# Performance work log

Measured on AMD Instinct MI355X. Metric: run time of the kernel, lower is better.

## Reference

```python
import jax, jax.numpy as jnp
import numpy as np

MARGIN = 0.075
CONF_THRESHOLD = 0.2


def setup_inputs() -> dict:
    key = jax.random.key(0)
    k1, k2, k3 = jax.random.split(key, 3)
    N, D = 32768, 256
    embeddings = jax.random.normal(k1, (N, D), dtype=jnp.float32)
    tags = jax.random.randint(k2, (N,), 0, 500, dtype=jnp.int64)
    confidences = jax.random.uniform(k3, (N,), dtype=jnp.float32)
    return {"embeddings": embeddings, "tags": tags, "confidences": confidences}


def _safe_sqrt(sq):
    # gradient-safe sqrt: zero at sq<=0 (matches d(0)=0, avoids NaN in vjp)
    pos = sq > 0
    return jnp.where(pos, jnp.sqrt(jnp.where(pos, sq, 1.0)), 0.0)


def _triplet_hard_mining(emb, labels):
    n = emb.shape[0]
    # pairwise euclidean distances (cdist p=2)
    sq_norm = jnp.sum(emb * emb, axis=1)  # [n]
    sq = sq_norm[:, None] + sq_norm[None, :] - 2.0 * (emb @ emb.T)
    dist = _safe_sqrt(jnp.maximum(sq, 0.0))  # [n, n]

    same = labels[:, None] == labels[None, :]
    eye = jnp.eye(n, dtype=bool)
    pos_mask = same & ~eye
    neg_mask = ~same

    inf = jnp.float32(jnp.inf)
    hard_pos = jnp.max(jnp.where(pos_mask, dist, -inf), axis=1)  # [n]
    neg_min = jnp.min(jnp.where(neg_mask, dist, inf), axis=1)    # [n]
    # semi-hard negatives: neg dists strictly greater than hardest positive
    shn_mask = neg_mask & (dist > hard_pos[:, None])
    shn_min = jnp.min(jnp.where(shn_mask, dist, inf), axis=1)
    hard_neg = jnp.where(jnp.isfinite(shn_min), shn_min, neg_min)

    valid = jnp.any(pos_mask, axis=1) & jnp.any(neg_mask, axis=1)
    per_anchor = jax.nn.relu(hard_pos - hard_neg + MARGIN)
    per_anchor = jnp.where(valid, per_anchor, 0.0)
    cnt = jnp.sum(valid.astype(jnp.float32))
    # if no valid anchors (also covers <2 unique labels), loss is 0
    return jnp.where(cnt > 0, jnp.sum(per_anchor) / jnp.maximum(cnt, 1.0), 0.0)


def reference(embeddings, tags, confidences):
    n = embeddings.shape[0]
    top_k = int(CONF_THRESHOLD * n)
    _, idx = jax.lax.top_k(confidences, top_k)
    emb = embeddings[idx]
    labels = tags[idx]
    return _triplet_hard_mining(emb, labels)
```

## Files before the change

kernel.cpp:

```cpp
#include <hip/hip_runtime.h>
#include <math.h>

#define D 256
#define MARGIN 0.075f
#define MAXM 96
#define NBIN 16384

typedef __bf16 bf8_t __attribute__((ext_vector_type(8)));
typedef float f4_t __attribute__((ext_vector_type(4)));
typedef unsigned long long ull;

#define AS1 __attribute__((address_space(1)))
#define AS3 __attribute__((address_space(3)))
static __device__ __forceinline__ void gload_lds16(const void* g, void* s) {
    __builtin_amdgcn_global_load_lds((const AS1 unsigned int*)g, (AS3 unsigned int*)s, 16, 0, 0);
}

#define ALOADU(p) __hip_atomic_load((p), __ATOMIC_RELAXED, __HIP_MEMORY_SCOPE_AGENT)
#define ASTOREU(p, v) __hip_atomic_store((p), (v), __ATOMIC_RELAXED, __HIP_MEMORY_SCOPE_AGENT)

#define VDRAIN() asm volatile("s_waitcnt vmcnt(0)" ::: "memory")

static __device__ __forceinline__ unsigned short f2bf(float x) {
    unsigned u = __float_as_uint(x);
    unsigned r = (u + 0x7fffu + ((u >> 16) & 1u)) >> 16;
    return (unsigned short)r;
}

static __device__ __forceinline__ float dec_min(unsigned cm) {
    return (cm == 0u) ? __builtin_inff() : __uint_as_float(~cm);
}

static __device__ __forceinline__ float rmin16(float v) {
    int s;
    s = __builtin_amdgcn_update_dpp(__float_as_int(v), __float_as_int(v), 0x101, 0xF, 0xF, false);
    v = fminf(v, __int_as_float(s));
    s = __builtin_amdgcn_update_dpp(__float_as_int(v), __float_as_int(v), 0x102, 0xF, 0xF, false);
    v = fminf(v, __int_as_float(s));
    s = __builtin_amdgcn_update_dpp(__float_as_int(v), __float_as_int(v), 0x104, 0xF, 0xF, false);
    v = fminf(v, __int_as_float(s));
    s = __builtin_amdgcn_update_dpp(__float_as_int(v), __float_as_int(v), 0x108, 0xF, 0xF, false);
    v = fminf(v, __int_as_float(s));
    return v;
}

__global__ __launch_bounds__(1024) void k_hist(const float* __restrict__ conf, int n,
                                               unsigned* __restrict__ hist,
                                               unsigned* __restrict__ ctrl, int ksel) {
    int t = threadIdx.x;
    int i = blockIdx.x * 1024 + t;
    if (i < n) {
        unsigned b = __float_as_uint(conf[i]) >> 16;
        if (b > NBIN - 1u) b = NBIN - 1u;
        atomicAdd(&hist[b], 1u);
    }
    VDRAIN();
    __syncthreads();
    __shared__ int lastf;
    if (t == 0) lastf = (atomicAdd(&ctrl[10], 1u) == gridDim.x - 1) ? 1 : 0;
    __syncthreads();
    if (!lastf) return;

    __shared__ unsigned part[1024];
    __shared__ int schunk;
    unsigned k = (unsigned)ksel;
    unsigned loc[16];
    unsigned s = 0;
    #pragma unroll
    for (int b = 0; b < 16; b++) {
        loc[b] = ALOADU(&hist[t * 16 + b]);
        s += loc[b];
    }
    part[t] = s;
    __syncthreads();
    for (int off = 1; off < 1024; off <<= 1) {
        unsigned v = (t + off < 1024) ? part[t + off] : 0u;
        __syncthreads();
        part[t] += v;
        __syncthreads();
    }
    if (part[t] >= k && (t == 1023 || part[t + 1] < k)) schunk = t;
    __syncthreads();
    int c = schunk;
    if (t == c) {
        unsigned cum = (c == 1023) ? 0u : part[c + 1];
        int bin = 0; unsigned rem = 1;
        #pragma unroll
        for (int b = 15; b >= 0; b--) {
            unsigned h = loc[b];
            if (cum + h >= k) { bin = c * 16 + b; rem = k - cum; break; }
            cum += h;
        }
        ctrl[3] = (unsigned)bin;
        ctrl[1] = k - rem;
        ctrl[2] = rem;
    }
}

__global__ __launch_bounds__(1024) void k_sel(const float* __restrict__ conf, int n,
                                              unsigned* __restrict__ ctrl,
                                              int* __restrict__ idx_sel,
                                              ull* __restrict__ cand) {
    int t = threadIdx.x;
    int i = blockIdx.x * 1024 + t;
    unsigned b16 = ctrl[3];
    if (i < n) {
        unsigned u = __float_as_uint(conf[i]);
        unsigned t16 = u >> 16;
        if (t16 > NBIN - 1u) t16 = NBIN - 1u;
        if (t16 > b16) {
            unsigned pos = atomicAdd(&ctrl[5], 1u);
            idx_sel[pos] = i;
        } else if (t16 == b16) {
            unsigned pos = atomicAdd(&ctrl[6], 1u);
            ASTOREU(&cand[pos], ((ull)u << 32) | (unsigned)i);
        }
    }
    VDRAIN();
    __syncthreads();
    __shared__ int lastf;
    if (t == 0) lastf = (atomicAdd(&ctrl[11], 1u) == gridDim.x - 1) ? 1 : 0;
    __syncthreads();
    if (!lastf) return;

    __shared__ ull scand[2048];
    int M = (int)ALOADU(&ctrl[6]);
    unsigned need = ctrl[2], cgt = ctrl[1];
    if (M <= 2048) {
        for (int j = t; j < M; j += 1024) scand[j] = ALOADU(&cand[j]);
        __syncthreads();
        for (int j = t; j < M; j += 1024) {
            ull cj = scand[j];
            unsigned uj = (unsigned)(cj >> 32);
            unsigned rank = 0;
            for (int m = 0; m < M; m++) {
                ull cm = scand[m];
                unsigned um = (unsigned)(cm >> 32);
                if (um > uj || (um == uj && cm < cj)) rank++;
            }
            if (rank < need) idx_sel[cgt + rank] = (int)(unsigned)(cj & 0xFFFFFFFFu);
        }
    } else {
        for (int j = t; j < M; j += 1024) {
            ull cj = ALOADU(&cand[j]);
            unsigned uj = (unsigned)(cj >> 32);
            unsigned rank = 0;
            for (int m = 0; m < M; m++) {
                ull cm = ALOADU(&cand[m]);
                unsigned um = (unsigned)(cm >> 32);
                if (um > uj || (um == uj && cm < cj)) rank++;
            }
            if (rank < need) idx_sel[cgt + rank] = (int)(unsigned)(cj & 0xFFFFFFFFu);
        }
    }
}

__global__ __launch_bounds__(256) void k_gather(const float* __restrict__ emb,
                                                const int* __restrict__ tags,
                                                const int* __restrict__ idx_sel,
                                                int ksel, int np,
                                                unsigned short* __restrict__ ebf,
                                                float* __restrict__ sqn,
                                                int* __restrict__ lsel,
                                                unsigned* __restrict__ labhist,
                                                int* __restrict__ members) {
    int j = blockIdx.x * 4 + (threadIdx.x >> 6);
    int t = threadIdx.x & 63;
    if (j < ksel) {
        int src = idx_sel[j];
        float4 v = *(const float4*)&emb[(size_t)src * D + t * 4];
        ushort4 o;
        o.x = f2bf(v.x); o.y = f2bf(v.y); o.z = f2bf(v.z); o.w = f2bf(v.w);
        *(ushort4*)&ebf[(size_t)j * D + t * 4] = o;
        float s = v.x * v.x + v.y * v.y + v.z * v.z + v.w * v.w;
        for (int off = 32; off > 0; off >>= 1) s += __shfl_down(s, off);
        if (t == 0) {
            int lab = tags[src];
            sqn[j] = s; lsel[j] = lab;
            unsigned slot = atomicAdd(&labhist[lab], 1u);
            if (slot < MAXM) members[lab * MAXM + slot] = j;
        }
    } else if (j < np) {
        ushort4 z = {0, 0, 0, 0};
        *(ushort4*)&ebf[(size_t)j * D + t * 4] = z;
        if (t == 0) { sqn[j] = __builtin_inff(); lsel[j] = -1; }
    }
}

__global__ __launch_bounds__(256) void k_hardpos(const unsigned short* __restrict__ ebf,
                                                 const float* __restrict__ sqn,
                                                 const int* __restrict__ members,
                                                 const unsigned* __restrict__ labhist,
                                                 unsigned* __restrict__ hp_g) {
    int L = blockIdx.x;
    int t = threadIdx.x;
    int m = (int)labhist[L];
    if (m > MAXM) m = MAXM;
    if (m < 2) return;

    __shared__ unsigned short rows[MAXM * 256];
    __shared__ float lsqn[MAXM];
    __shared__ unsigned hpl[MAXM];
    __shared__ int ridx[MAXM];

    for (int a = t; a < m; a += 256) {
        int r = members[L * MAXM + a];
        ridx[a] = r; lsqn[a] = sqn[r]; hpl[a] = 0u;
    }
    __syncthreads();
    for (int e = t * 8; e < m * 256; e += 256 * 8) {
        int a = e >> 8, c = e & 255;
        *(uint4*)&rows[a * 256 + c] = *(const uint4*)&ebf[(size_t)ridx[a] * D + c];
    }
    __syncthreads();

    int npair = m * (m - 1) / 2;
    for (int pidx = t; pidx < npair; pidx += 256) {
        int a = 0, rem = pidx;
        while (rem >= m - 1 - a) { rem -= m - 1 - a; a++; }
        int b = a + 1 + rem;
        const unsigned* ra = (const unsigned*)&rows[a * 256];
        const unsigned* rb = (const unsigned*)&rows[b * 256];
        float dot = 0.f;
        #pragma unroll 8
        for (int c = 0; c < 128; c++) {
            unsigned ua = ra[c], ub = rb[c];
            float a0 = __uint_as_float(ua << 16);
            float a1 = __uint_as_float(ua & 0xFFFF0000u);
            float b0 = __uint_as_float(ub << 16);
            float b1 = __uint_as_float(ub & 0xFFFF0000u);
            dot = fmaf(a0, b0, dot);
            dot = fmaf(a1, b1, dot);
        }
        float dsq = fmaxf(lsqn[a] + lsqn[b] - 2.f * dot, 0.f);
        unsigned bits = __float_as_uint(dsq);
        atomicMax(&hpl[a], bits);
        atomicMax(&hpl[b], bits);
    }
    __syncthreads();
    for (int a = t; a < m; a += 256) hp_g[ridx[a]] = hpl[a];
}

__global__ __launch_bounds__(256, 2) void k_fused(const unsigned short* __restrict__ Ebf,
                                                  const float* __restrict__ sqn,
                                                  const int* __restrict__ lsel,
                                                  const unsigned* __restrict__ hp_g,
                                                  unsigned* __restrict__ nm_g,
                                                  unsigned* __restrict__ shn_g,
                                                  const unsigned* __restrict__ labhist,
                                                  unsigned* __restrict__ ctrl,
                                                  float* __restrict__ out,
                                                  int np, int nb, int ksel, int ntri) {
    int rem = blockIdx.x, bi = 0;
    while (rem >= nb - bi) { rem -= nb - bi; bi++; }
    int bj = bi + rem;
    int i0 = bi * 128, j0 = bj * 128;
    bool diag = (bi == bj);

    __shared__ __align__(16) char smem[65536];

    int t = threadIdx.x;
    int w = t >> 6, l = t & 63;
    int wm = w & 1, wn = w >> 1;
    int lr = l & 15, lq = l >> 4;
    int r7 = lr & 7, rh = lr >> 3;

    int dr = l >> 3;
    int sg = (l & 7) ^ dr;
    const unsigned short* gA = Ebf + (size_t)(i0 + dr) * D + sg * 8;
    const unsigned short* gB = Ebf + (size_t)(j0 + dr) * D + sg * 8;

    f4_t zero = {0.f, 0.f, 0.f, 0.f};
    f4_t acc[4][4];
    #pragma unroll
    for (int p = 0; p < 4; p++)
        #pragma unroll
        for (int q = 0; q < 4; q++) acc[p][q] = zero;

    #pragma unroll
    for (int c = 0; c < 4; c++) {
        int R0 = w * 32 + c * 8;
        gload_lds16(gA + (size_t)R0 * D, smem + R0 * 128);
        gload_lds16(gB + (size_t)R0 * D, smem + 16384 + R0 * 128);
    }

    #pragma unroll
    for (int tt = 0; tt < 4; ++tt) {
        char* cb = smem + ((tt & 1) << 15);
        __syncthreads();
        if (tt < 3) {
            char* nb_ = smem + (((tt + 1) & 1) << 15);
            int ko = (tt + 1) * 64;
            #pragma unroll
            for (int c = 0; c < 4; c++) {
                int R0 = w * 32 + c * 8;
                gload_lds16(gA + (size_t)R0 * D + ko, nb_ + R0 * 128);
                gload_lds16(gB + (size_t)R0 * D + ko, nb_ + 16384 + R0 * 128);
            }
        }
        #pragma unroll
        for (int ks8 = 0; ks8 < 8; ks8 += 4) {
            bf8_t a[4], b[4];
            #pragma unroll
            for (int p = 0; p < 4; p++) {
                int off = ((wm * 8 + p * 2 + rh) << 10) + ((r7 * 8 + ((ks8 + lq) ^ r7)) << 4);
                a[p] = *(const bf8_t*)(cb + off);
            }
            #pragma unroll
            for (int q = 0; q < 4; q++) {
                int off = ((wn * 8 + q * 2 + rh) << 10) + ((r7 * 8 + ((ks8 + lq) ^ r7)) << 4);
                b[q] = *(const bf8_t*)(cb + 16384 + off);
            }
            #pragma unroll
            for (int p = 0; p < 4; p++)
                #pragma unroll
                for (int q = 0; q < 4; q++)
                    acc[p][q] = __builtin_amdgcn_mfma_f32_16x16x32_bf16(a[p], b[q], acc[p][q], 0, 0, 0);
        }
    }

    float* sqnA = (float*)smem;
    float* sqnB = sqnA + 128;
    int* labA = (int*)(sqnB + 128);
    int* labB = labA + 128;
    float* hpA2 = (float*)(labB + 128);
    float* hpB2 = hpA2 + 128;
    if (t < 128) {
        sqnA[t] = sqn[i0 + t];
        labA[t] = lsel[i0 + t];
        hpA2[t] = __uint_as_float(hp_g[i0 + t]);
    } else {
        int u = t - 128;
        sqnB[u] = sqn[j0 + u];
        labB[u] = lsel[j0 + u];
        hpB2[u] = __uint_as_float(hp_g[j0 + u]);
    }
    __syncthreads();

    const float INF = __builtin_inff();
    float dsq[4][4][4];
    int colL[4], ljv[4];
    float sBv[4];
    #pragma unroll
    for (int q = 0; q < 4; q++) {
        colL[q] = wn * 64 + q * 16 + lr;
        ljv[q] = labB[colL[q]];
        sBv[q] = sqnB[colL[q]];
    }
    #pragma unroll
    for (int p = 0; p < 4; p++) {
        #pragma unroll
        for (int r = 0; r < 4; r++) {
            int rowL = wm * 64 + p * 16 + lq * 4 + r;
            float smi = sqnA[rowL];
            #pragma unroll
            for (int q = 0; q < 4; q++)
                dsq[p][q][r] = fmaxf(smi + sBv[q] - 2.f * acc[p][q][r], 0.f);
        }
    }

    #pragma unroll
    for (int p = 0; p < 4; p++) {
        #pragma unroll
        for (int r = 0; r < 4; r++) {
            int rowL = wm * 64 + p * 16 + lq * 4 + r;
            int li = labA[rowL];
            float hpr = hpA2[rowL];
            float nmv = INF, smv = INF;
            #pragma unroll
            for (int q = 0; q < 4; q++) {
                float d = dsq[p][q][r];
                if (ljv[q] != li) {
                    nmv = fminf(nmv, d);
                    if (d > hpr) smv = fminf(smv, d);
                }
            }
            nmv = rmin16(nmv);
            smv = rmin16(smv);
            if (lr == 0) {
                if (nmv < INF) atomicMax(&nm_g[i0 + rowL], ~__float_as_uint(nmv));
                if (smv < INF) atomicMax(&shn_g[i0 + rowL], ~__float_as_uint(smv));
            }
        }
    }

    if (!diag) {
        #pragma unroll
        for (int q = 0; q < 4; q++) {
            int lj = ljv[q];
            float hpc = hpB2[colL[q]];
            float nmv = INF, smv = INF;
            #pragma unroll
            for (int p = 0; p < 4; p++)
                #pragma unroll
                for (int r = 0; r < 4; r++) {
                    int rowL = wm * 64 + p * 16 + lq * 4 + r;
                    float d = dsq[p][q][r];
                    if (labA[rowL] != lj) {
                        nmv = fminf(nmv, d);
                        if (d > hpc) smv = fminf(smv, d);
                    }
                }
            nmv = fminf(nmv, __shfl_xor(nmv, 16));
            nmv = fminf(nmv, __shfl_xor(nmv, 32));
            smv = fminf(smv, __shfl_xor(smv, 16));
            smv = fminf(smv, __shfl_xor(smv, 32));
            if (lq == 0) {
                if (nmv < INF) atomicMax(&nm_g[j0 + colL[q]], ~__float_as_uint(nmv));
                if (smv < INF) atomicMax(&shn_g[j0 + colL[q]], ~__float_as_uint(smv));
            }
        }
    }

    VDRAIN();
    __syncthreads();
    __shared__ int lastf;
    if (t == 0) lastf = (atomicAdd(&ctrl[8], 1u) == (unsigned)(ntri - 1)) ? 1 : 0;
    __syncthreads();
    if (!lastf) return;

    float sum = 0.f, cnt = 0.f;
    for (int i = t; i < ksel; i += 256) {
        int li = lsel[i];
        unsigned h = labhist[li];
        bool valid = (h >= 2u) && ((unsigned)ksel > h);
        if (valid) {
            float hp2 = __uint_as_float(hp_g[i]);
            float nm2 = dec_min(ALOADU(&nm_g[i]));
            float sh2 = dec_min(ALOADU(&shn_g[i]));
            float hn2 = isinf(sh2) ? nm2 : sh2;
            sum += fmaxf(sqrtf(hp2) - sqrtf(hn2) + MARGIN, 0.f);
            cnt += 1.f;
        }
    }
    float* ssum = (float*)smem;
    float* scnt = ssum + 256;
    ssum[t] = sum; scnt[t] = cnt;
    __syncthreads();
    for (int off = 128; off > 0; off >>= 1) {
        if (t < off) { ssum[t] += ssum[t + off]; scnt[t] += scnt[t + off]; }
        __syncthreads();
    }
    if (t == 0) {
        float s = ssum[0], c = scnt[0];
        out[0] = (c > 0.f) ? (s / fmaxf(c, 1.f)) : 0.f;
    }
}

__global__ void k_wsfail(float* out, float code) { out[0] = code; }

static inline size_t align_up(size_t x, size_t a) { return (x + a - 1) & ~(a - 1); }

extern "C" void kernel_launch(void* const* d_in, const int* in_sizes, int n_in,
                              void* d_out, int out_size, void* d_ws, size_t ws_size,
                              hipStream_t stream) {
    const float* emb  = (const float*)d_in[0];
    const int*   tags = (const int*)d_in[1];
    const float* conf = (const float*)d_in[2];
    float* out = (float*)d_out;

    int n = in_sizes[2];
    int ksel = (int)(0.2 * (double)n);
    int np = ((ksel + 127) / 128) * 128;
    int nb = np / 128;
    int nlab = 512;

    size_t off = 0;
    size_t o_ctrl = off; off = align_up(off + 32 * sizeof(unsigned), 256);
    size_t o_lh   = off; off = align_up(off + (size_t)nlab * 4, 256);
    size_t o_hp   = off; off = align_up(off + (size_t)np * 4, 256);
    size_t o_nm   = off; off = align_up(off + (size_t)np * 4, 256);
    size_t o_shn  = off; off = align_up(off + (size_t)np * 4, 256);
    size_t o_h1   = off; off = align_up(off + (size_t)NBIN * 4, 256);
    size_t zero_bytes = off;
    size_t o_idx  = off; off = align_up(off + (size_t)ksel * 4, 256);
    size_t o_cand = off; off = align_up(off + (size_t)n * 8, 256);
    size_t o_mem  = off; off = align_up(off + (size_t)nlab * MAXM * 4, 256);
    size_t o_lab  = off; off = align_up(off + (size_t)np * 4, 256);
    size_t o_sqn  = off; off = align_up(off + (size_t)np * 4, 256);
    size_t o_ebf  = off; off = align_up(off + (size_t)np * D * 2, 256);

    if (ws_size < off) {
        k_wsfail<<<1, 1, 0, stream>>>(out, -(float)(ws_size >> 20));
        return;
    }

    char* ws = (char*)d_ws;
    unsigned*       ctrl    = (unsigned*)(ws + o_ctrl);
    unsigned*       labhist = (unsigned*)(ws + o_lh);
    unsigned*       hp_g    = (unsigned*)(ws + o_hp);
    unsigned*       nm_g    = (unsigned*)(ws + o_nm);
    unsigned*       shn_g   = (unsigned*)(ws + o_shn);
    unsigned*       h1      = (unsigned*)(ws + o_h1);
    int*            idx_sel = (int*)(ws + o_idx);
    ull*            cand    = (ull*)(ws + o_cand);
    int*            members = (int*)(ws + o_mem);
    int*            lsel    = (int*)(ws + o_lab);
    float*          sqn     = (float*)(ws + o_sqn);
    unsigned short* ebf     = (unsigned short*)(ws + o_ebf);

    hipMemsetAsync(d_ws, 0, zero_bytes, stream);
    int nhb = (n + 1023) / 1024;
    k_hist<<<nhb, 1024, 0, stream>>>(conf, n, h1, ctrl, ksel);
    k_sel<<<nhb, 1024, 0, stream>>>(conf, n, ctrl, idx_sel, cand);
    k_gather<<<np / 4, 256, 0, stream>>>(emb, tags, idx_sel, ksel, np, ebf, sqn, lsel,
                                         labhist, members);
    k_hardpos<<<512, 256, 0, stream>>>(ebf, sqn, members, labhist, hp_g);
    int ntri = nb * (nb + 1) / 2;
    k_fused<<<ntri, 256, 0, stream>>>(ebf, sqn, lsel, hp_g, nm_g, shn_g, labhist, ctrl,
                                      out, np, nb, ksel, ntri);
}
```

Measured before the change: 207.5 us.

## Use 512-thread blocks with single-buffered LDS in fused distance kernel

The fused pairwise-distance/mining kernel now runs 8 waves per 128x128 tile instead of 4, so each wave computes a 64x32 sub-tile with half the accumulators. LDS drops from a 64KB double buffer to a 32KB single buffer, with load-then-compute-then-sync per K chunk. The aim is higher occupancy (launch bounds 512,6) so that more concurrent blocks hide latency. In exchange, the prefetch overlap of the next K chunk is lost and each tile needs extra barriers.

```diff
diff --git a/kernel.cpp b/kernel.cpp
--- a/kernel.cpp
+++ b/kernel.cpp
@@ -241,7 +241,7 @@
     for (int a = t; a < m; a += 256) hp_g[ridx[a]] = hpl[a];
 }
 
-__global__ __launch_bounds__(256, 2) void k_fused(const unsigned short* __restrict__ Ebf,
+__global__ __launch_bounds__(512, 6) void k_fused(const unsigned short* __restrict__ Ebf,
                                                   const float* __restrict__ sqn,
                                                   const int* __restrict__ lsel,
                                                   const unsigned* __restrict__ hp_g,
@@ -257,11 +257,14 @@
     int i0 = bi * 128, j0 = bj * 128;
     bool diag = (bi == bj);
 
-    __shared__ __align__(16) char smem[65536];
+    __shared__ __align__(16) char smem[32768];
+    char* ldsA = smem;
+    char* ldsB = smem + 16384;
 
     int t = threadIdx.x;
     int w = t >> 6, l = t & 63;
-    int wm = w & 1, wn = w >> 1;
+    int wm = w >> 2;
+    int wn = w & 3;
     int lr = l & 15, lq = l >> 4;
     int r7 = lr & 7, rh = lr >> 3;
 
@@ -271,52 +274,40 @@
     const unsigned short* gB = Ebf + (size_t)(j0 + dr) * D + sg * 8;
 
     f4_t zero = {0.f, 0.f, 0.f, 0.f};
-    f4_t acc[4][4];
+    f4_t acc[4][2];
     #pragma unroll
     for (int p = 0; p < 4; p++)
         #pragma unroll
-        for (int q = 0; q < 4; q++) acc[p][q] = zero;
-
-    #pragma unroll
-    for (int c = 0; c < 4; c++) {
-        int R0 = w * 32 + c * 8;
-        gload_lds16(gA + (size_t)R0 * D, smem + R0 * 128);
-        gload_lds16(gB + (size_t)R0 * D, smem + 16384 + R0 * 128);
-    }
-
-    #pragma unroll
-    for (int tt = 0; tt < 4; ++tt) {
-        char* cb = smem + ((tt & 1) << 15);
+        for (int q = 0; q < 2; q++) acc[p][q] = zero;
+
+    for (int k0 = 0; k0 < D; k0 += 64) {
+        #pragma unroll
+        for (int c = 0; c < 2; c++) {
+            int R0 = w * 16 + c * 8;
+            gload_lds16(gA + (size_t)R0 * D + k0, ldsA + R0 * 128);
+            gload_lds16(gB + (size_t)R0 * D + k0, ldsB + R0 * 128);
+        }
         __syncthreads();
-        if (tt < 3) {
-            char* nb_ = smem + (((tt + 1) & 1) << 15);
-            int ko = (tt + 1) * 64;
-            #pragma unroll
-            for (int c = 0; c < 4; c++) {
-                int R0 = w * 32 + c * 8;
-                gload_lds16(gA + (size_t)R0 * D + ko, nb_ + R0 * 128);
-                gload_lds16(gB + (size_t)R0 * D + ko, nb_ + 16384 + R0 * 128);
-            }
-        }
         #pragma unroll
         for (int ks8 = 0; ks8 < 8; ks8 += 4) {
-            bf8_t a[4], b[4];
+            bf8_t a[4], b[2];
             #pragma unroll
             for (int p = 0; p < 4; p++) {
                 int off = ((wm * 8 + p * 2 + rh) << 10) + ((r7 * 8 + ((ks8 + lq) ^ r7)) << 4);
-                a[p] = *(const bf8_t*)(cb + off);
+                a[p] = *(const bf8_t*)(ldsA + off);
             }
             #pragma unroll
-            for (int q = 0; q < 4; q++) {
-                int off = ((wn * 8 + q * 2 + rh) << 10) + ((r7 * 8 + ((ks8 + lq) ^ r7)) << 4);
-                b[q] = *(const bf8_t*)(cb + 16384 + off);
+            for (int q = 0; q < 2; q++) {
+                int off = ((wn * 4 + q * 2 + rh) << 10) + ((r7 * 8 + ((ks8 + lq) ^ r7)) << 4);
+                b[q] = *(const bf8_t*)(ldsB + off);
             }
             #pragma unroll
             for (int p = 0; p < 4; p++)
                 #pragma unroll
-                for (int q = 0; q < 4; q++)
+                for (int q = 0; q < 2; q++)
                     acc[p][q] = __builtin_amdgcn_mfma_f32_16x16x32_bf16(a[p], b[q], acc[p][q], 0, 0, 0);
         }
+        __syncthreads();
     }
 
     float* sqnA = (float*)smem;
@@ -329,7 +320,7 @@
         sqnA[t] = sqn[i0 + t];
         labA[t] = lsel[i0 + t];
         hpA2[t] = __uint_as_float(hp_g[i0 + t]);
-    } else {
+    } else if (t < 256) {
         int u = t - 128;
         sqnB[u] = sqn[j0 + u];
         labB[u] = lsel[j0 + u];
@@ -338,12 +329,12 @@
     __syncthreads();
 
     const float INF = __builtin_inff();
-    float dsq[4][4][4];
-    int colL[4], ljv[4];
-    float sBv[4];
+    float dsq[4][2][4];
+    int colL[2], ljv[2];
+    float sBv[2];
     #pragma unroll
-    for (int q = 0; q < 4; q++) {
-        colL[q] = wn * 64 + q * 16 + lr;
+    for (int q = 0; q < 2; q++) {
+        colL[q] = wn * 32 + q * 16 + lr;
         ljv[q] = labB[colL[q]];
         sBv[q] = sqnB[colL[q]];
     }
@@ -354,7 +345,7 @@
             int rowL = wm * 64 + p * 16 + lq * 4 + r;
             float smi = sqnA[rowL];
             #pragma unroll
-            for (int q = 0; q < 4; q++)
+            for (int q = 0; q < 2; q++)
                 dsq[p][q][r] = fmaxf(smi + sBv[q] - 2.f * acc[p][q][r], 0.f);
         }
     }
@@ -368,7 +359,7 @@
             float hpr = hpA2[rowL];
             float nmv = INF, smv = INF;
             #pragma unroll
-            for (int q = 0; q < 4; q++) {
+            for (int q = 0; q < 2; q++) {
                 float d = dsq[p][q][r];
                 if (ljv[q] != li) {
                     nmv = fminf(nmv, d);
@@ -386,7 +377,7 @@
 
     if (!diag) {
         #pragma unroll
-        for (int q = 0; q < 4; q++) {
+        for (int q = 0; q < 2; q++) {
             int lj = ljv[q];
             float hpc = hpB2[colL[q]];
             float nmv = INF, smv = INF;
@@ -420,7 +411,7 @@
     if (!lastf) return;
 
     float sum = 0.f, cnt = 0.f;
-    for (int i = t; i < ksel; i += 256) {
+    for (int i = t; i < ksel; i += 512) {
         int li = lsel[i];
         unsigned h = labhist[li];
         bool valid = (h >= 2u) && ((unsigned)ksel > h);
@@ -434,10 +425,10 @@
         }
     }
     float* ssum = (float*)smem;
-    float* scnt = ssum + 256;
+    float* scnt = ssum + 512;
     ssum[t] = sum; scnt[t] = cnt;
     __syncthreads();
-    for (int off = 128; off > 0; off >>= 1) {
+    for (int off = 256; off > 0; off >>= 1) {
         if (t < off) { ssum[t] += ssum[t + off]; scnt[t] += scnt[t + off]; }
         __syncthreads();
     }
@@ -507,6 +498,6 @@
                                          labhist, members);
     k_hardpos<<<512, 256, 0, stream>>>(ebf, sqn, members, labhist, hp_g);
     int ntri = nb * (nb + 1) / 2;
-    k_fused<<<ntri, 256, 0, stream>>>(ebf, sqn, lsel, hp_g, nm_g, shn_g, labhist, ctrl,
+    k_fused<<<ntri, 512, 0, stream>>>(ebf, sqn, lsel, hp_g, nm_g, shn_g, labhist, ctrl,
                                       out, np, nb, ksel, ntri);
 }
```

Measured after the change: 207.3 us. Within noise of the previous version (-0.1%).

## Load MFMA operands directly from global memory instead of LDS double-buffering

Applied to the files above, without the earlier changes.

Removes the LDS-staged, double-buffered global_load_lds pipeline for the 128x128 bf16 Gram tile and has each wave read its A/B fragments straight from global memory (relying on L1/L2 reuse). Shared memory shrinks from 64KB to 4KB and launch bounds are raised to allow 4 blocks per CU, aiming for more occupancy to hide latency. The cost is more redundant global and cache traffic, since the waves sharing a row or column block each fetch it themselves, and the loop no longer overlaps prefetch with compute.

```diff
diff --git a/kernel.cpp b/kernel.cpp
--- a/kernel.cpp
+++ b/kernel.cpp
@@ -9,12 +9,6 @@
 typedef __bf16 bf8_t __attribute__((ext_vector_type(8)));
 typedef float f4_t __attribute__((ext_vector_type(4)));
 typedef unsigned long long ull;
-
-#define AS1 __attribute__((address_space(1)))
-#define AS3 __attribute__((address_space(3)))
-static __device__ __forceinline__ void gload_lds16(const void* g, void* s) {
-    __builtin_amdgcn_global_load_lds((const AS1 unsigned int*)g, (AS3 unsigned int*)s, 16, 0, 0);
-}
 
 #define ALOADU(p) __hip_atomic_load((p), __ATOMIC_RELAXED, __HIP_MEMORY_SCOPE_AGENT)
 #define ASTOREU(p, v) __hip_atomic_store((p), (v), __ATOMIC_RELAXED, __HIP_MEMORY_SCOPE_AGENT)
@@ -241,7 +235,7 @@
     for (int a = t; a < m; a += 256) hp_g[ridx[a]] = hpl[a];
 }
 
-__global__ __launch_bounds__(256, 2) void k_fused(const unsigned short* __restrict__ Ebf,
+__global__ __launch_bounds__(256, 4) void k_fused(const unsigned short* __restrict__ Ebf,
                                                   const float* __restrict__ sqn,
                                                   const int* __restrict__ lsel,
                                                   const unsigned* __restrict__ hp_g,
@@ -257,18 +251,15 @@
     int i0 = bi * 128, j0 = bj * 128;
     bool diag = (bi == bj);
 
-    __shared__ __align__(16) char smem[65536];
+    __shared__ __align__(16) char smem[4096];
 
     int t = threadIdx.x;
     int w = t >> 6, l = t & 63;
     int wm = w & 1, wn = w >> 1;
     int lr = l & 15, lq = l >> 4;
-    int r7 = lr & 7, rh = lr >> 3;
-
-    int dr = l >> 3;
-    int sg = (l & 7) ^ dr;
-    const unsigned short* gA = Ebf + (size_t)(i0 + dr) * D + sg * 8;
-    const unsigned short* gB = Ebf + (size_t)(j0 + dr) * D + sg * 8;
+
+    const unsigned short* aBase = Ebf + (size_t)(i0 + wm * 64 + lr) * D + lq * 8;
+    const unsigned short* bBase = Ebf + (size_t)(j0 + wn * 64 + lr) * D + lq * 8;
 
     f4_t zero = {0.f, 0.f, 0.f, 0.f};
     f4_t acc[4][4];
@@ -278,39 +269,16 @@
         for (int q = 0; q < 4; q++) acc[p][q] = zero;
 
     #pragma unroll
-    for (int c = 0; c < 4; c++) {
-        int R0 = w * 32 + c * 8;
-        gload_lds16(gA + (size_t)R0 * D, smem + R0 * 128);
-        gload_lds16(gB + (size_t)R0 * D, smem + 16384 + R0 * 128);
-    }
-
-    #pragma unroll
-    for (int tt = 0; tt < 4; ++tt) {
-        char* cb = smem + ((tt & 1) << 15);
-        __syncthreads();
-        if (tt < 3) {
-            char* nb_ = smem + (((tt + 1) & 1) << 15);
-            int ko = (tt + 1) * 64;
-            #pragma unroll
-            for (int c = 0; c < 4; c++) {
-                int R0 = w * 32 + c * 8;
-                gload_lds16(gA + (size_t)R0 * D + ko, nb_ + R0 * 128);
-                gload_lds16(gB + (size_t)R0 * D + ko, nb_ + 16384 + R0 * 128);
-            }
-        }
+    for (int k0 = 0; k0 < D; k0 += 64) {
         #pragma unroll
         for (int ks8 = 0; ks8 < 8; ks8 += 4) {
             bf8_t a[4], b[4];
             #pragma unroll
-            for (int p = 0; p < 4; p++) {
-                int off = ((wm * 8 + p * 2 + rh) << 10) + ((r7 * 8 + ((ks8 + lq) ^ r7)) << 4);
-                a[p] = *(const bf8_t*)(cb + off);
-            }
-            #pragma unroll
-            for (int q = 0; q < 4; q++) {
-                int off = ((wn * 8 + q * 2 + rh) << 10) + ((r7 * 8 + ((ks8 + lq) ^ r7)) << 4);
-                b[q] = *(const bf8_t*)(cb + 16384 + off);
-            }
+            for (int p = 0; p < 4; p++)
+                a[p] = *(const bf8_t*)(aBase + p * (16 * D) + k0 + ks8 * 8);
+            #pragma unroll
+            for (int q = 0; q < 4; q++)
+                b[q] = *(const bf8_t*)(bBase + q * (16 * D) + k0 + ks8 * 8);
             #pragma unroll
             for (int p = 0; p < 4; p++)
                 #pragma unroll
```

Result: slower. 236.9 us (+14.2%).
